# Kernel tuning notes

Measured on AMD Instinct MI355X. Metric: run time of the kernel, lower is better.

Reference implementation:

```python
import jax, jax.numpy as jnp
import numpy as np

N_NODES = 50000
N_EDGES = 800000
IN_F = 128
OUT_F = 64
ORDER = 3


def _spmm(edge_index, edge_attr, x):
    # out[row] += edge_attr[e] * x[col]  (COO sparse @ dense)
    row, col = edge_index[0], edge_index[1]
    msgs = x[col] * edge_attr[:, None]          # [E, F] gather + scale
    return jax.ops.segment_sum(msgs, row, num_segments=N_NODES)  # scatter-add


def setup_inputs() -> dict:
    key = jax.random.key(0)
    k1, k2, k3, k4 = jax.random.split(key, 4)
    x = jax.random.normal(k1, (N_NODES, IN_F), dtype=jnp.float32)
    edge_index = jax.random.randint(k2, (2, N_EDGES), 0, N_NODES, dtype=jnp.int64)
    edge_attr = jax.random.uniform(k3, (N_EDGES,), dtype=jnp.float32)
    W = jax.random.normal(k4, (OUT_F, IN_F), dtype=jnp.float32) * (1.0 / np.sqrt(IN_F))
    b = jnp.zeros((OUT_F,), dtype=jnp.float32)
    return {"x": x, "edge_index": edge_index, "edge_attr": edge_attr, "W": W, "b": b}


def reference(x, edge_index, edge_attr, W, b):
    # output = Linear(x); then `order` rounds of spmm aggregation
    out = jnp.einsum("ni,oi->no", x, W) + b      # [N, OUT_F]
    for _ in range(ORDER):
        out = _spmm(edge_index, edge_attr, out)
    return out
```

## Files before the change

kernel.cpp:

```cpp
#include <hip/hip_runtime.h>

#define IN_F   128
#define OUT_F  64
#define GR     64
#define EPB    4096

__device__ __forceinline__ unsigned short f2bf(float f) {
    unsigned int u = __float_as_uint(f);
    u += 0x7fffu + ((u >> 16) & 1u);
    return (unsigned short)(u >> 16);
}
__device__ __forceinline__ float bf2f(unsigned short h) {
    return __uint_as_float(((unsigned int)h) << 16);
}

template <bool BF16OUT>
__global__ __launch_bounds__(256) void gemm_kernel(
    const float* __restrict__ x, const float* __restrict__ W,
    const float* __restrict__ b, void* __restrict__ outv, int N) {
    __shared__ float xs[GR][IN_F + 4];
    __shared__ float Wt[IN_F][OUT_F + 4];

    const int t = threadIdx.x;
    const int row0 = blockIdx.x * GR;

    for (int i = t; i < OUT_F * (IN_F / 4); i += 256) {
        int o = i & 63;
        int c = i >> 6;
        float4 v = ((const float4*)W)[o * (IN_F / 4) + c];
        Wt[4 * c + 0][o] = v.x;
        Wt[4 * c + 1][o] = v.y;
        Wt[4 * c + 2][o] = v.z;
        Wt[4 * c + 3][o] = v.w;
    }
    for (int i = t; i < GR * (IN_F / 4); i += 256) {
        int r = i >> 5, c = i & 31;
        int gr = row0 + r;
        float4 v = make_float4(0.f, 0.f, 0.f, 0.f);
        if (gr < N) v = ((const float4*)x)[(size_t)gr * (IN_F / 4) + c];
        *(float4*)&xs[r][4 * c] = v;
    }
    __syncthreads();

    const int f0 = (t & 15) * 4;
    const int r0 = (t >> 4) * 4;
    float acc[4][4] = {};

    #pragma unroll 2
    for (int k = 0; k < IN_F; k += 4) {
        float4 xv[4], wv[4];
        #pragma unroll
        for (int i = 0; i < 4; ++i) xv[i] = *(const float4*)&xs[r0 + i][k];
        #pragma unroll
        for (int j = 0; j < 4; ++j) wv[j] = *(const float4*)&Wt[k + j][f0];
        #pragma unroll
        for (int i = 0; i < 4; ++i) {
            #pragma unroll
            for (int j = 0; j < 4; ++j) {
                float wx = j == 0 ? wv[0].x : (j == 1 ? wv[0].y : (j == 2 ? wv[0].z : wv[0].w));
                float wy = j == 0 ? wv[1].x : (j == 1 ? wv[1].y : (j == 2 ? wv[1].z : wv[1].w));
                float wz = j == 0 ? wv[2].x : (j == 1 ? wv[2].y : (j == 2 ? wv[2].z : wv[2].w));
                float ww = j == 0 ? wv[3].x : (j == 1 ? wv[3].y : (j == 2 ? wv[3].z : wv[3].w));
                acc[i][j] = fmaf(xv[i].x, wx, acc[i][j]);
                acc[i][j] = fmaf(xv[i].y, wy, acc[i][j]);
                acc[i][j] = fmaf(xv[i].z, wz, acc[i][j]);
                acc[i][j] = fmaf(xv[i].w, ww, acc[i][j]);
            }
        }
    }

    float4 bv = *(const float4*)&b[f0];
    #pragma unroll
    for (int i = 0; i < 4; ++i) {
        int gr = row0 + r0 + i;
        if (gr < N) {
            float o0 = acc[i][0] + bv.x, o1 = acc[i][1] + bv.y;
            float o2 = acc[i][2] + bv.z, o3 = acc[i][3] + bv.w;
            if (BF16OUT) {
                ushort4 u = { f2bf(o0), f2bf(o1), f2bf(o2), f2bf(o3) };
                *(ushort4*)((unsigned short*)outv + (size_t)gr * OUT_F + f0) = u;
            } else {
                float4 o4 = make_float4(o0, o1, o2, o3);
                *(float4*)((float*)outv + (size_t)gr * OUT_F + f0) = o4;
            }
        }
    }
}

__global__ __launch_bounds__(256) void bhist_kernel(const int* __restrict__ rowi,
                                                    int* __restrict__ bcnt, int E) {
    __shared__ int cnt[256];
    int t = threadIdx.x;
    cnt[t] = 0;
    __syncthreads();
    for (int e = blockIdx.x * 256 + t; e < E; e += gridDim.x * 256)
        atomicAdd(&cnt[rowi[e] >> 8], 1);
    __syncthreads();
    if (cnt[t] > 0) atomicAdd(&bcnt[t], cnt[t]);
}

__global__ __launch_bounds__(256) void bscan_kernel(const int* __restrict__ bcnt,
                                                    int* __restrict__ bbase,
                                                    int* __restrict__ bcursor,
                                                    int* __restrict__ rowptr,
                                                    int nb, int N, int E) {
    int t = threadIdx.x;
    int v = (t < nb) ? bcnt[t] : 0;
    int lane = t & 63, w = t >> 6;
    int sum = v;
    #pragma unroll
    for (int off = 1; off < 64; off <<= 1) {
        int x = __shfl_up(sum, off, 64);
        if (lane >= off) sum += x;
    }
    __shared__ int wsum[4];
    if (lane == 63) wsum[w] = sum;
    __syncthreads();
    int woff = 0;
    for (int i = 0; i < w; ++i) woff += wsum[i];
    int excl = sum + woff - v;
    if (t <= nb) bbase[t] = excl;
    if (t < nb)  bcursor[t] = excl;
    if (t == 0)  rowptr[N] = E;
}

__global__ __launch_bounds__(256) void bin_kernel(
    const int* __restrict__ rowi, const int* __restrict__ coli,
    const float* __restrict__ attr, int* __restrict__ bcursor,
    unsigned long long* __restrict__ tmp, int E) {
    __shared__ int cnt[256];
    __shared__ int cur[256];
    __shared__ int gbase[256];
    int t = threadIdx.x;
    int e0 = blockIdx.x * EPB;
    cnt[t] = 0;
    cur[t] = 0;
    __syncthreads();
    int myrow[16];
    #pragma unroll
    for (int i = 0; i < 16; ++i) {
        int e = e0 + i * 256 + t;
        myrow[i] = (e < E) ? rowi[e] : -1;
        if (myrow[i] >= 0) atomicAdd(&cnt[myrow[i] >> 8], 1);
    }
    __syncthreads();
    if (cnt[t] > 0) gbase[t] = atomicAdd(&bcursor[t], cnt[t]);
    __syncthreads();
    #pragma unroll
    for (int i = 0; i < 16; ++i) {
        int e = e0 + i * 256 + t;
        if (myrow[i] >= 0) {
            int b = myrow[i] >> 8;
            int rank = atomicAdd(&cur[b], 1);
            unsigned long long rec = ((unsigned long long)(myrow[i] & 255) << 32)
                                   | ((unsigned int)coli[e] << 16)
                                   | (unsigned int)f2bf(attr[e]);
            tmp[(size_t)gbase[b] + rank] = rec;
        }
    }
}

__global__ __launch_bounds__(256) void bsort_kernel(
    const unsigned long long* __restrict__ tmp, const int* __restrict__ bbase,
    unsigned int* __restrict__ scv, int* __restrict__ rowptr, int N) {
    __shared__ int cnt[256];
    __shared__ int cur[256];
    __shared__ int wsum[4];
    int t = threadIdx.x, b = blockIdx.x;
    int seg = bbase[b], segend = bbase[b + 1];
    cnt[t] = 0;
    __syncthreads();
    for (int i = seg + t; i < segend; i += 256)
        atomicAdd(&cnt[(int)(tmp[i] >> 32)], 1);
    __syncthreads();
    int v = cnt[t];
    int lane = t & 63, w = t >> 6;
    int sum = v;
    #pragma unroll
    for (int off = 1; off < 64; off <<= 1) {
        int x = __shfl_up(sum, off, 64);
        if (lane >= off) sum += x;
    }
    if (lane == 63) wsum[w] = sum;
    __syncthreads();
    int woff = 0;
    for (int i = 0; i < w; ++i) woff += wsum[i];
    int excl = sum + woff - v;
    int gidx = b * 256 + t;
    if (gidx <= N) rowptr[gidx] = seg + excl;
    cur[t] = excl;
    __syncthreads();
    for (int i = seg + t; i < segend; i += 256) {
        unsigned long long rec = tmp[i];
        int rl = (int)(rec >> 32);
        int pos = atomicAdd(&cur[rl], 1);
        scv[(size_t)seg + pos] = (unsigned int)rec;
    }
}

template <bool BF16OUT>
__global__ __launch_bounds__(256) void spmm_csr_kernel(
    const int* __restrict__ rowptr, const unsigned int* __restrict__ scv,
    const unsigned short* __restrict__ in, void* __restrict__ outv, int N) {
    int wid = (blockIdx.x * 256 + threadIdx.x) >> 6;
    int lane = threadIdx.x & 63;
    if (wid >= N) return;
    wid = __builtin_amdgcn_readfirstlane(wid);
    int beg = rowptr[wid], end = rowptr[wid + 1];
    float acc = 0.f;
    int e = beg;
    for (; e + 16 <= end; e += 16) {
        unsigned int v[16];
        #pragma unroll
        for (int i = 0; i < 16; ++i) v[i] = scv[e + i];
        float xv[16];
        #pragma unroll
        for (int i = 0; i < 16; ++i) xv[i] = bf2f(in[(size_t)(v[i] >> 16) * OUT_F + lane]);
        #pragma unroll
        for (int i = 0; i < 16; ++i) acc = fmaf(bf2f((unsigned short)(v[i] & 0xffffu)), xv[i], acc);
    }
    for (; e + 4 <= end; e += 4) {
        unsigned int v[4];
        #pragma unroll
        for (int i = 0; i < 4; ++i) v[i] = scv[e + i];
        float xv[4];
        #pragma unroll
        for (int i = 0; i < 4; ++i) xv[i] = bf2f(in[(size_t)(v[i] >> 16) * OUT_F + lane]);
        #pragma unroll
        for (int i = 0; i < 4; ++i) acc = fmaf(bf2f((unsigned short)(v[i] & 0xffffu)), xv[i], acc);
    }
    for (; e < end; ++e) {
        unsigned int v = scv[e];
        acc = fmaf(bf2f((unsigned short)(v & 0xffffu)),
                   bf2f(in[(size_t)(v >> 16) * OUT_F + lane]), acc);
    }
    if (BF16OUT)
        ((unsigned short*)outv)[(size_t)wid * OUT_F + lane] = f2bf(acc);
    else
        ((float*)outv)[(size_t)wid * OUT_F + lane] = acc;
}

__global__ __launch_bounds__(256) void spmm_atomic_kernel(
    const int* __restrict__ rowi, const int* __restrict__ coli,
    const float* __restrict__ attr, const float* __restrict__ in,
    float* __restrict__ out, int E) {
    int tid = blockIdx.x * 256 + threadIdx.x;
    int e = tid >> 6;
    int lane = tid & 63;
    if (e >= E) return;
    int r = rowi[e];
    int c = coli[e];
    float w = attr[e];
    float v = in[(size_t)c * OUT_F + lane];
    atomicAdd(&out[(size_t)r * OUT_F + lane], w * v);
}

extern "C" void kernel_launch(void* const* d_in, const int* in_sizes, int n_in,
                              void* d_out, int out_size, void* d_ws, size_t ws_size,
                              hipStream_t stream) {
    const float* x    = (const float*)d_in[0];
    const int*   ei   = (const int*)d_in[1];
    const float* attr = (const float*)d_in[2];
    const float* W    = (const float*)d_in[3];
    const float* b    = (const float*)d_in[4];
    float* out = (float*)d_out;

    const int N = in_sizes[0] / IN_F;
    const int E = in_sizes[2];
    const int* rowi = ei;
    const int* coli = ei + E;

    const size_t obytes_f  = (size_t)N * OUT_F * sizeof(float);
    const size_t obytes_bf = (size_t)N * OUT_F * sizeof(unsigned short);
    const int nb = (N + 255) / 256;

    char* wp = (char*)d_ws;
    size_t off = 0;
    auto alloc = [&](size_t bytes) { char* p = wp + off; off += (bytes + 255) & ~(size_t)255; return p; };
    unsigned short* bufA = (unsigned short*)alloc(obytes_bf);
    unsigned short* bufB = (unsigned short*)alloc((size_t)E * 8);
    unsigned long long* tmp = (unsigned long long*)bufB;
    int* rowptr  = (int*)alloc((size_t)(N + 1) * 4);
    int* bcnt    = (int*)alloc(260 * 4);
    int* bbase   = (int*)alloc(260 * 4);
    int* bcursor = (int*)alloc(260 * 4);
    unsigned int* scv = (unsigned int*)alloc((size_t)E * 4);
    const bool csr_ok = (off <= ws_size) && (N <= 65280) && ((size_t)E * 8 >= obytes_bf);

    const int gemm_blocks = (N + GR - 1) / GR;
    const int sb = (N * 64 + 255) / 256;

    if (csr_ok) {
        gemm_kernel<true><<<gemm_blocks, 256, 0, stream>>>(x, W, b, bufA, N);

        hipMemsetAsync(bcnt, 0, 260 * 4, stream);
        bhist_kernel<<<512, 256, 0, stream>>>(rowi, bcnt, E);
        bscan_kernel<<<1, 256, 0, stream>>>(bcnt, bbase, bcursor, rowptr, nb, N, E);
        bin_kernel<<<(E + EPB - 1) / EPB, 256, 0, stream>>>(rowi, coli, attr, bcursor, tmp, E);
        bsort_kernel<<<nb, 256, 0, stream>>>(tmp, bbase, scv, rowptr, N);

        spmm_csr_kernel<true ><<<sb, 256, 0, stream>>>(rowptr, scv, bufA, bufB, N);
        spmm_csr_kernel<true ><<<sb, 256, 0, stream>>>(rowptr, scv, bufB, bufA, N);
        spmm_csr_kernel<false><<<sb, 256, 0, stream>>>(rowptr, scv, bufA, out, N);
    } else {
        float* ws0 = (float*)d_ws;
        gemm_kernel<false><<<gemm_blocks, 256, 0, stream>>>(x, W, b, ws0, N);
        const int spmm_blocks = (E * 64 + 255) / 256;
        hipMemsetAsync(out, 0, obytes_f, stream);
        spmm_atomic_kernel<<<spmm_blocks, 256, 0, stream>>>(rowi, coli, attr, ws0, out, E);
        hipMemsetAsync(ws0, 0, obytes_f, stream);
        spmm_atomic_kernel<<<spmm_blocks, 256, 0, stream>>>(rowi, coli, attr, out, ws0, E);
        hipMemsetAsync(out, 0, obytes_f, stream);
        spmm_atomic_kernel<<<spmm_blocks, 256, 0, stream>>>(rowi, coli, attr, ws0, out, E);
    }
}
```

Baseline: 201.0 us.

## Use bf16 MFMA for linear layer and half-wave paired-edge SpMM gathers

The linear layer GEMM now converts x and W to bf16 in LDS and computes with 16x16x32 bf16 MFMA instructions, staging the bf16 output through LDS for coalesced stores. The CSR SpMM kernel now has each half-wave process alternate edges, with every lane gathering two packed bf16 features as one 32-bit load, and the two halves are combined with a cross-lane shuffle. This aims to cut GEMM ALU time and to halve gather instruction count while doubling edge-level parallelism per wave. Inputs to the GEMM are rounded to bf16, which lowers precision compared with the fp32 FMA path.

```diff
diff --git a/kernel.cpp b/kernel.cpp
--- a/kernel.cpp
+++ b/kernel.cpp
@@ -2,8 +2,10 @@
 
 #define IN_F   128
 #define OUT_F  64
-#define GR     64
 #define EPB    4096
+
+typedef __attribute__((ext_vector_type(8))) short bf16x8;
+typedef __attribute__((ext_vector_type(4))) float f32x4;
 
 __device__ __forceinline__ unsigned short f2bf(float f) {
     unsigned int u = __float_as_uint(f);
@@ -18,72 +20,72 @@
 __global__ __launch_bounds__(256) void gemm_kernel(
     const float* __restrict__ x, const float* __restrict__ W,
     const float* __restrict__ b, void* __restrict__ outv, int N) {
-    __shared__ float xs[GR][IN_F + 4];
-    __shared__ float Wt[IN_F][OUT_F + 4];
-
+    __shared__ unsigned short lds[2 * 64 * 136];
     const int t = threadIdx.x;
-    const int row0 = blockIdx.x * GR;
-
-    for (int i = t; i < OUT_F * (IN_F / 4); i += 256) {
-        int o = i & 63;
-        int c = i >> 6;
-        float4 v = ((const float4*)W)[o * (IN_F / 4) + c];
-        Wt[4 * c + 0][o] = v.x;
-        Wt[4 * c + 1][o] = v.y;
-        Wt[4 * c + 2][o] = v.z;
-        Wt[4 * c + 3][o] = v.w;
-    }
-    for (int i = t; i < GR * (IN_F / 4); i += 256) {
-        int r = i >> 5, c = i & 31;
-        int gr = row0 + r;
+    const int w = t >> 6;
+    const int lane = t & 63;
+    const int row0 = blockIdx.x * 64;
+
+    #pragma unroll
+    for (int it = 0; it < 8; ++it) {
+        int flat = it * 256 + t;
+        int r = flat >> 5, c = flat & 31;
         float4 v = make_float4(0.f, 0.f, 0.f, 0.f);
-        if (gr < N) v = ((const float4*)x)[(size_t)gr * (IN_F / 4) + c];
-        *(float4*)&xs[r][4 * c] = v;
-    }
-    __syncthreads();
-
-    const int f0 = (t & 15) * 4;
-    const int r0 = (t >> 4) * 4;
-    float acc[4][4] = {};
-
-    #pragma unroll 2
-    for (int k = 0; k < IN_F; k += 4) {
-        float4 xv[4], wv[4];
-        #pragma unroll
-        for (int i = 0; i < 4; ++i) xv[i] = *(const float4*)&xs[r0 + i][k];
-        #pragma unroll
-        for (int j = 0; j < 4; ++j) wv[j] = *(const float4*)&Wt[k + j][f0];
-        #pragma unroll
-        for (int i = 0; i < 4; ++i) {
+        if (row0 + r < N) v = ((const float4*)x)[(size_t)(row0 + r) * 32 + c];
+        ushort4 u = { f2bf(v.x), f2bf(v.y), f2bf(v.z), f2bf(v.w) };
+        *(ushort4*)&lds[r * 136 + c * 4] = u;
+    }
+    #pragma unroll
+    for (int it = 0; it < 8; ++it) {
+        int flat = it * 256 + t;
+        int o = flat >> 5, c = flat & 31;
+        float4 v = ((const float4*)W)[(size_t)o * 32 + c];
+        ushort4 u = { f2bf(v.x), f2bf(v.y), f2bf(v.z), f2bf(v.w) };
+        *(ushort4*)&lds[64 * 136 + o * 136 + c * 4] = u;
+    }
+    __syncthreads();
+
+    const int m = lane & 15;
+    const int quad = lane >> 4;
+    f32x4 acc[4] = {};
+    #pragma unroll
+    for (int kb = 0; kb < 4; ++kb) {
+        bf16x8 af = *(const bf16x8*)&lds[(w * 16 + m) * 136 + kb * 32 + quad * 8];
+        #pragma unroll
+        for (int ot = 0; ot < 4; ++ot) {
+            bf16x8 bf = *(const bf16x8*)&lds[64 * 136 + (ot * 16 + m) * 136 + kb * 32 + quad * 8];
+            acc[ot] = __builtin_amdgcn_mfma_f32_16x16x32_bf16(af, bf, acc[ot], 0, 0, 0);
+        }
+    }
+
+    float bv[4];
+    #pragma unroll
+    for (int ot = 0; ot < 4; ++ot) bv[ot] = b[ot * 16 + m];
+
+    __syncthreads();
+    if (BF16OUT) {
+        #pragma unroll
+        for (int ot = 0; ot < 4; ++ot)
             #pragma unroll
-            for (int j = 0; j < 4; ++j) {
-                float wx = j == 0 ? wv[0].x : (j == 1 ? wv[0].y : (j == 2 ? wv[0].z : wv[0].w));
-                float wy = j == 0 ? wv[1].x : (j == 1 ? wv[1].y : (j == 2 ? wv[1].z : wv[1].w));
-                float wz = j == 0 ? wv[2].x : (j == 1 ? wv[2].y : (j == 2 ? wv[2].z : wv[2].w));
-                float ww = j == 0 ? wv[3].x : (j == 1 ? wv[3].y : (j == 2 ? wv[3].z : wv[3].w));
-                acc[i][j] = fmaf(xv[i].x, wx, acc[i][j]);
-                acc[i][j] = fmaf(xv[i].y, wy, acc[i][j]);
-                acc[i][j] = fmaf(xv[i].z, wz, acc[i][j]);
-                acc[i][j] = fmaf(xv[i].w, ww, acc[i][j]);
+            for (int reg = 0; reg < 4; ++reg)
+                lds[(w * 16 + quad * 4 + reg) * 72 + ot * 16 + m] = f2bf(acc[ot][reg] + bv[ot]);
+        __syncthreads();
+        #pragma unroll
+        for (int it = 0; it < 4; ++it) {
+            int flat = it * 256 + t;
+            int r = flat >> 4, c4 = flat & 15;
+            if (row0 + r < N)
+                *(ushort4*)((unsigned short*)outv + (size_t)(row0 + r) * 64 + c4 * 4)
+                    = *(ushort4*)&lds[r * 72 + c4 * 4];
+        }
+    } else {
+        #pragma unroll
+        for (int ot = 0; ot < 4; ++ot)
+            #pragma unroll
+            for (int reg = 0; reg < 4; ++reg) {
+                int rr = row0 + w * 16 + quad * 4 + reg;
+                if (rr < N) ((float*)outv)[(size_t)rr * 64 + ot * 16 + m] = acc[ot][reg] + bv[ot];
             }
-        }
-    }
-
-    float4 bv = *(const float4*)&b[f0];
-    #pragma unroll
-    for (int i = 0; i < 4; ++i) {
-        int gr = row0 + r0 + i;
-        if (gr < N) {
-            float o0 = acc[i][0] + bv.x, o1 = acc[i][1] + bv.y;
-            float o2 = acc[i][2] + bv.z, o3 = acc[i][3] + bv.w;
-            if (BF16OUT) {
-                ushort4 u = { f2bf(o0), f2bf(o1), f2bf(o2), f2bf(o3) };
-                *(ushort4*)((unsigned short*)outv + (size_t)gr * OUT_F + f0) = u;
-            } else {
-                float4 o4 = make_float4(o0, o1, o2, o3);
-                *(float4*)((float*)outv + (size_t)gr * OUT_F + f0) = o4;
-            }
-        }
     }
 }
 
@@ -201,43 +203,52 @@
 template <bool BF16OUT>
 __global__ __launch_bounds__(256) void spmm_csr_kernel(
     const int* __restrict__ rowptr, const unsigned int* __restrict__ scv,
-    const unsigned short* __restrict__ in, void* __restrict__ outv, int N) {
+    const unsigned int* __restrict__ in32, void* __restrict__ outv, int N) {
     int wid = (blockIdx.x * 256 + threadIdx.x) >> 6;
     int lane = threadIdx.x & 63;
     if (wid >= N) return;
     wid = __builtin_amdgcn_readfirstlane(wid);
     int beg = rowptr[wid], end = rowptr[wid + 1];
-    float acc = 0.f;
+    int half = lane >> 5;
+    int lh = lane & 31;
+    float accx = 0.f, accy = 0.f;
     int e = beg;
     for (; e + 16 <= end; e += 16) {
-        unsigned int v[16];
-        #pragma unroll
-        for (int i = 0; i < 16; ++i) v[i] = scv[e + i];
-        float xv[16];
-        #pragma unroll
-        for (int i = 0; i < 16; ++i) xv[i] = bf2f(in[(size_t)(v[i] >> 16) * OUT_F + lane]);
-        #pragma unroll
-        for (int i = 0; i < 16; ++i) acc = fmaf(bf2f((unsigned short)(v[i] & 0xffffu)), xv[i], acc);
-    }
-    for (; e + 4 <= end; e += 4) {
-        unsigned int v[4];
-        #pragma unroll
-        for (int i = 0; i < 4; ++i) v[i] = scv[e + i];
-        float xv[4];
-        #pragma unroll
-        for (int i = 0; i < 4; ++i) xv[i] = bf2f(in[(size_t)(v[i] >> 16) * OUT_F + lane]);
-        #pragma unroll
-        for (int i = 0; i < 4; ++i) acc = fmaf(bf2f((unsigned short)(v[i] & 0xffffu)), xv[i], acc);
-    }
-    for (; e < end; ++e) {
-        unsigned int v = scv[e];
-        acc = fmaf(bf2f((unsigned short)(v & 0xffffu)),
-                   bf2f(in[(size_t)(v >> 16) * OUT_F + lane]), acc);
-    }
-    if (BF16OUT)
-        ((unsigned short*)outv)[(size_t)wid * OUT_F + lane] = f2bf(acc);
-    else
-        ((float*)outv)[(size_t)wid * OUT_F + lane] = acc;
+        unsigned int rec[16];
+        #pragma unroll
+        for (int i = 0; i < 16; ++i) rec[i] = scv[e + i];
+        unsigned int xp[8]; float wv[8];
+        #pragma unroll
+        for (int p = 0; p < 8; ++p) {
+            unsigned int r = half ? rec[2 * p + 1] : rec[2 * p];
+            wv[p] = __uint_as_float(r << 16);
+            xp[p] = in32[(size_t)(r >> 16) * 32 + lh];
+        }
+        #pragma unroll
+        for (int p = 0; p < 8; ++p) {
+            accx = fmaf(wv[p], __uint_as_float(xp[p] << 16), accx);
+            accy = fmaf(wv[p], __uint_as_float(xp[p] & 0xffff0000u), accy);
+        }
+    }
+    for (; e < end; e += 2) {
+        unsigned int rA = scv[e];
+        unsigned int rB = (e + 1 < end) ? scv[e + 1] : 0u;
+        unsigned int r = half ? rB : rA;
+        float w = __uint_as_float(r << 16);
+        unsigned int xpv = in32[(size_t)(r >> 16) * 32 + lh];
+        accx = fmaf(w, __uint_as_float(xpv << 16), accx);
+        accy = fmaf(w, __uint_as_float(xpv & 0xffff0000u), accy);
+    }
+    accx += __shfl_xor(accx, 32, 64);
+    accy += __shfl_xor(accy, 32, 64);
+    if (half == 0) {
+        if (BF16OUT) {
+            unsigned int o = (unsigned int)f2bf(accx) | ((unsigned int)f2bf(accy) << 16);
+            ((unsigned int*)outv)[(size_t)wid * 32 + lh] = o;
+        } else {
+            ((float2*)outv)[(size_t)wid * 32 + lh] = make_float2(accx, accy);
+        }
+    }
 }
 
 __global__ __launch_bounds__(256) void spmm_atomic_kernel(
@@ -287,7 +298,7 @@
     unsigned int* scv = (unsigned int*)alloc((size_t)E * 4);
     const bool csr_ok = (off <= ws_size) && (N <= 65280) && ((size_t)E * 8 >= obytes_bf);
 
-    const int gemm_blocks = (N + GR - 1) / GR;
+    const int gemm_blocks = (N + 63) / 64;
     const int sb = (N * 64 + 255) / 256;
 
     if (csr_ok) {
@@ -299,9 +310,9 @@
         bin_kernel<<<(E + EPB - 1) / EPB, 256, 0, stream>>>(rowi, coli, attr, bcursor, tmp, E);
         bsort_kernel<<<nb, 256, 0, stream>>>(tmp, bbase, scv, rowptr, N);
 
-        spmm_csr_kernel<true ><<<sb, 256, 0, stream>>>(rowptr, scv, bufA, bufB, N);
-        spmm_csr_kernel<true ><<<sb, 256, 0, stream>>>(rowptr, scv, bufB, bufA, N);
-        spmm_csr_kernel<false><<<sb, 256, 0, stream>>>(rowptr, scv, bufA, out, N);
+        spmm_csr_kernel<true ><<<sb, 256, 0, stream>>>(rowptr, scv, (const unsigned int*)bufA, bufB, N);
+        spmm_csr_kernel<true ><<<sb, 256, 0, stream>>>(rowptr, scv, (const unsigned int*)bufB, bufA, N);
+        spmm_csr_kernel<false><<<sb, 256, 0, stream>>>(rowptr, scv, (const unsigned int*)bufA, out, N);
     } else {
         float* ws0 = (float*)d_ws;
         gemm_kernel<false><<<gemm_blocks, 256, 0, stream>>>(x, W, b, ws0, N);
```

Result: slower. 279.1 us (+38.9%).
